# Optimization experiments

Measured on AMD Instinct MI355X. Metric: run time of the kernel, lower is better.

## Reference

```python
import jax, jax.numpy as jnp
import numpy as np

B, C3, H3, W3 = 8, 512, 24, 24
C5, H5, W5 = 256, 96, 96
GRIDS = (6, 3, 2, 1)
GROUPS = 2


def conv2d(x, w):
    # stride-1 'same' conv (matches torch autopad k//2 for odd k), NCHW/OIHW
    return jax.lax.conv_general_dilated(x, w, (1, 1), 'SAME',
                                        dimension_numbers=('NCHW', 'OIHW', 'NCHW'))


def conv_bn_silu(x, w):
    # ultralytics-style Conv = Conv2d(bias=False) + BatchNorm2d + SiLU.
    # BN in eval with default running stats (mean=0, var=1, gamma=1, beta=0) is identity.
    return jax.nn.silu(conv2d(x, w))


def psp(x):
    # adaptive_avg_pool2d to (g, g) for each grid; H,W divisible by all grids -> equal bins
    b, c, h, w = x.shape
    outs = []
    for g in GRIDS:
        outs.append(x.reshape(b, c, g, h // g, g, w // g).mean(axis=(3, 5)).reshape(b, c, g * g))
    return jnp.concatenate(outs, axis=2)  # [b, c, 36+9+4+1=50]


def resize_bilinear_ac(x, oh, ow):
    # F.interpolate(mode='bilinear', align_corners=True)
    n, c, h, w = x.shape
    ys = jnp.linspace(0.0, h - 1.0, oh)
    xs = jnp.linspace(0.0, w - 1.0, ow)
    y0 = jnp.clip(jnp.floor(ys).astype(jnp.int32), 0, h - 2)
    x0 = jnp.clip(jnp.floor(xs).astype(jnp.int32), 0, w - 2)
    wy = (ys - y0)[None, None, :, None]
    wx = (xs - x0)[None, None, None, :]
    xr = jnp.take(x, y0, axis=2) * (1 - wy) + jnp.take(x, y0 + 1, axis=2) * wy
    return jnp.take(xr, x0, axis=3) * (1 - wx) + jnp.take(xr, x0 + 1, axis=3) * wx


def grid_sample(img, grid):
    # F.grid_sample bilinear, align_corners=True, padding_mode='zeros'
    # img [N,C,H,W], grid [N,Ho,Wo,2] with (x,y) normalized coords
    n, c, h, w = img.shape
    gx = (grid[..., 0] + 1.0) * 0.5 * (w - 1)
    gy = (grid[..., 1] + 1.0) * 0.5 * (h - 1)
    x0 = jnp.floor(gx)
    y0 = jnp.floor(gy)
    wx1 = gx - x0
    wy1 = gy - y0
    flat = img.reshape(n, c, h * w)

    def gather(xi, yi, wgt):
        valid = (xi >= 0) & (xi <= w - 1) & (yi >= 0) & (yi <= h - 1)
        xc = jnp.clip(xi, 0, w - 1).astype(jnp.int32)
        yc = jnp.clip(yi, 0, h - 1).astype(jnp.int32)
        idx = (yc * w + xc).reshape(n, 1, -1)
        v = jnp.take_along_axis(flat, idx, axis=2).reshape(n, c, grid.shape[1], grid.shape[2])
        return v * (wgt * valid)[:, None]

    return (gather(x0, y0, (1 - wx1) * (1 - wy1)) + gather(x0 + 1, y0, wx1 * (1 - wy1))
            + gather(x0, y0 + 1, (1 - wx1) * wy1) + gather(x0 + 1, y0 + 1, wx1 * wy1))


def _w(key, shape):
    fan_in = int(np.prod(shape[1:]))
    return (jax.random.normal(key, shape, jnp.float32) / np.sqrt(fan_in)).astype(jnp.float32)


def setup_inputs() -> dict:
    key = jax.random.key(0)
    ks = jax.random.split(key, 17)
    return {
        'p3': jax.random.normal(ks[0], (B, C3, H3, W3), jnp.float32),
        'p5': jax.random.normal(ks[1], (B, C5, H5, W5), jnp.float32),
        # CFC_CRB
        'w_red': _w(ks[2], (C3, C3, 3, 3)),
        'wq': _w(ks[3], (32, C3, 1, 1)), 'bq': jnp.zeros((32,), jnp.float32),
        'wk': _w(ks[4], (32, C3)), 'bk': jnp.zeros((32,), jnp.float32),
        'wv': _w(ks[5], (C3, C3)), 'bv': jnp.zeros((C3,), jnp.float32),
        'la_w1': _w(ks[6], (C3 // 8, C3, 1, 1)),
        'la_w2': _w(ks[7], (C3, C3 // 8, 3, 3)),
        # SFC_G2
        'w32': _w(ks[8], (C5, C3, 3, 3)),
        'w8': _w(ks[9], (C5, C5, 3, 3)),
        'woff1': _w(ks[10], (64, 2 * C5, 1, 1)),
        'woff2': _w(ks[11], (GROUPS * 4 + 2, 64, 3, 3)),
    }


def reference(p3, p5, w_red, wq, bq, wk, bk, wv, bv, la_w1, la_w2, w32, w8, woff1, woff2):
    # ---------------- CFC_CRB ----------------
    x = conv_bn_silu(p3, w_red)                      # [b,512,h,w]
    b, c, h, w = x.shape
    q = conv2d(x, wq) + bq[None, :, None, None]       # [b,32,h,w]
    q = q.reshape(b, 32, h * w).transpose(0, 2, 1)    # [b,N,32]
    kfeat = psp(x)                                    # [b,512,50]
    k = jnp.einsum('oc,bcm->bom', wk, kfeat) + bk[None, :, None]   # [b,32,50]
    sim = jax.nn.softmax(jnp.einsum('bnc,bcm->bnm', q, k), axis=-1)  # [b,N,50]
    v = jnp.einsum('oc,bcm->bom', wv, kfeat) + bv[None, :, None]   # [b,512,50]
    context = jnp.einsum('bcm,bnm->bcn', v, sim).reshape(b, c, h, w)
    # LocalAttenModule: res1 * tanh(conv(context)) + res2
    mask = jnp.tanh(conv2d(conv_bn_silu(context, la_w1), la_w2))
    context = context * mask + context
    p3o = x + context                                 # [b,512,24,24]

    # ---------------- SFC_G2 ----------------
    sp = conv_bn_silu(p3o, w32)                       # [b,256,24,24]
    sp = resize_bilinear_ac(sp, H5, W5)               # [b,256,96,96]
    cp = conv_bn_silu(p5, w8)                         # [b,256,96,96]
    cr = conv2d(conv_bn_silu(jnp.concatenate([cp, sp], axis=1), woff1), woff2)  # [b,10,96,96]

    n = b
    spg = sp.reshape(n * GROUPS, -1, H5, W5)
    cpg = cp.reshape(n * GROUPS, -1, H5, W5)
    off_l = cr[:, 0:GROUPS * 2].reshape(n * GROUPS, 2, H5, W5)
    off_h = cr[:, GROUPS * 2:GROUPS * 4].reshape(n * GROUPS, 2, H5, W5)

    gx = jnp.linspace(-1.0, 1.0, W5)
    gy = jnp.linspace(-1.0, 1.0, H5)
    X, Y = jnp.meshgrid(gx, gy)                       # [H5,W5] each
    base = jnp.stack([X, Y], axis=-1)[None]           # [1,H5,W5,2] (x,y)
    norm = jnp.array([W5, H5], dtype=sp.dtype)
    grid_l = base + off_l.transpose(0, 2, 3, 1) / norm
    grid_h = base + off_h.transpose(0, 2, 3, 1) / norm

    cps = grid_sample(cpg, grid_l).reshape(n, -1, H5, W5)
    sps = grid_sample(spg, grid_h).reshape(n, -1, H5, W5)
    att = 1.0 + jnp.tanh(cr[:, GROUPS * 4:])          # [b,2,H,W]
    p5o = sps * att[:, 0:1] + cps * att[:, 1:2]
    return (p3o, p5o)
```

## Files before the change

### kernel.cpp

```cpp
#include <hip/hip_runtime.h>
#include <math.h>

#define DI __device__ __forceinline__

typedef __attribute__((ext_vector_type(8))) short bf16x8;
typedef __attribute__((ext_vector_type(4))) float f32x4;

DI float silu_f(float v) { return v / (1.f + __expf(-v)); }
DI float4 ld4(const float* p) { return *reinterpret_cast<const float4*>(p); }
DI void st4(float* p, const float4& v) { *reinterpret_cast<float4*>(p) = v; }
DI unsigned short f2bf(float f) {
    unsigned u = __float_as_uint(f);
    unsigned r = (u + 0x7FFFu + ((u >> 16) & 1u)) >> 16;
    return (unsigned short)r;
}
DI float bf2f(unsigned short u) { return __uint_as_float(((unsigned)u) << 16); }

DI void gload_lds16(const unsigned short* g, unsigned short* l) {
    __builtin_amdgcn_global_load_lds(
        (const __attribute__((address_space(1))) void*)g,
        (__attribute__((address_space(3))) void*)l, 16, 0, 0);
}

__global__ void pack_w2_kernel(const float* __restrict__ w, unsigned short* __restrict__ pk,
                               int Ci, int Co, int COG) {
    int idx = blockIdx.x * 256 + threadIdx.x;
    int total = Ci * Co * 9;
    if (idx >= total) return;
    int cc = idx & 31;
    int t = idx >> 5;
    int col = t % COG; t /= COG;
    int dydx = t % 9;  t /= 9;
    int nCoG = Co / COG;
    int cog = t % nCoG;
    int ch = t / nCoG;
    int co = cog * COG + col;
    pk[idx] = f2bf(w[((size_t)co * Ci + (ch << 5) + cc) * 9 + dydx]);
}

__global__ void pack_w1_kernel(const float* __restrict__ w, unsigned short* __restrict__ pk) {
    int idx = blockIdx.x * 256 + threadIdx.x;
    if (idx >= 32768) return;
    int cc = idx & 31;
    int col = (idx >> 5) & 63;
    int ch = idx >> 11;
    pk[idx] = f2bf(w[(size_t)col * 512 + (ch << 5) + cc]);
}

__global__ void zero_halo_kernel(unsigned short* __restrict__ pk, int P, int Hp, int Wp) {
    int border = 2 * Wp + 2 * (Hp - 2);
    int idx = blockIdx.x * 256 + threadIdx.x;
    if (idx >= P * border) return;
    int i = idx % border;
    int p = idx / border;
    int y, x;
    if (i < Wp) { y = 0; x = i; }
    else if (i < 2 * Wp) { y = Hp - 1; x = i - Wp; }
    else if (i < 2 * Wp + (Hp - 2)) { y = i - 2 * Wp + 1; x = 0; }
    else { y = i - 2 * Wp - (Hp - 2) + 1; x = Wp - 1; }
    unsigned short* d = pk + (((size_t)p * Hp + y) * Wp + x) * 32;
    uint4 z = make_uint4(0, 0, 0, 0);
    *(uint4*)&d[0] = z; *(uint4*)&d[8] = z; *(uint4*)&d[16] = z; *(uint4*)&d[24] = z;
}

__global__ void pack_in_pad_kernel(const float* __restrict__ in, unsigned short* __restrict__ pk,
                                   int Ci, int H, int W, int total) {
    int idx = blockIdx.x * 256 + threadIdx.x;
    if (idx >= total) return;
    const int nCh = Ci >> 5;
    const int HW = H * W;
    int cg = idx & 3;
    int t = idx >> 2;
    int pix = t % HW; t /= HW;
    int ch = t % nCh;
    int b = t / nCh;
    int y = pix / W, x = pix % W;
    const float* src = in + ((size_t)b * Ci + (ch << 5) + (cg << 3)) * HW + pix;
    unsigned p[4];
#pragma unroll
    for (int j = 0; j < 4; ++j) {
        float v0 = src[(size_t)(2 * j) * HW];
        float v1 = src[(size_t)(2 * j + 1) * HW];
        p[j] = (unsigned)f2bf(v0) | ((unsigned)f2bf(v1) << 16);
    }
    size_t dst = (((size_t)b * nCh + ch) * (H + 2) + (y + 1)) * (W + 2) + (x + 1);
    *(uint4*)&pk[dst * 32 + (cg << 3)] = make_uint4(p[0], p[1], p[2], p[3]);
}

template <int TH, int TW, int BF, int WCO, int FUSE, int OUTPK, int OUTPAD, int DBUF>
__global__ void __launch_bounds__(256)
conv3x3_mfma3(const unsigned short* __restrict__ pin, const unsigned short* __restrict__ wpk,
              float* __restrict__ out, unsigned short* __restrict__ outpk,
              int B, int Ci, int Co, int H, int W,
              const float* __restrict__ ctx, const float* __restrict__ xres) {
    static_assert(TH * TW == 4 * BF * 16, "tile px = 4 waves * BF frags * 16");
    constexpr int COG = WCO * 16;
    constexpr int TWH = TW + 2;
    constexpr int HP = (TH + 2) * TWH;
    constexpr int NG = HP * 4;
    constexpr int NIT = (NG + 255) / 256;
    static_assert(NG % 8 == 0, "granules divisible by 8");
    __shared__ __align__(16) unsigned short lin[NG * 8 * (DBUF + 1)];

    const int nTx = W / TW, nTy = H / TH, nCoG = Co / COG;
    const int Wp = W + 2, Hp = H + 2;
    const int nwg = gridDim.x;
    int wg = (blockIdx.x & 7) * (nwg >> 3) + (blockIdx.x >> 3);
    const int cog = wg % nCoG; wg /= nCoG;
    const int tx = wg % nTx;   wg /= nTx;
    const int ty = wg % nTy;
    const int b = wg / nTy;
    const int ox = tx * TW, oy = ty * TH, co0 = cog * COG;

    const int tid = threadIdx.x;
    const int lane = tid & 63;
    const int l15 = lane & 15, g = lane >> 4;
    const int wpx = (tid >> 6) * (BF * 16);

    int rr[BF], cc_[BF];
#pragma unroll
    for (int bf = 0; bf < BF; ++bf) {
        int px = wpx + bf * 16 + l15;
        rr[bf] = px / TW;
        cc_[bf] = px % TW;
    }

    f32x4 acc[WCO][BF];
#pragma unroll
    for (int af = 0; af < WCO; ++af)
#pragma unroll
        for (int bf = 0; bf < BF; ++bf) acc[af][bf] = {};

    const int nCh = Ci >> 5;
    const size_t HWs = (size_t)H * W;
    const size_t HpWp = (size_t)Hp * Wp;

    auto stage = [&](int ch, int buf) {
        const unsigned short* srcb = pin + ((size_t)b * nCh + ch) * HpWp * 32;
        unsigned short* dst = lin + buf * (NG * 8);
#pragma unroll
        for (int it = 0; it < NIT; ++it) {
            int s = it * 256 + tid;
            if (s < NG) {
                int e = s ^ ((s >> 3) & 7);
                int hp = e >> 2, cgp = e & 3;
                int hy = hp / TWH, hx = hp - hy * TWH;
                gload_lds16(srcb + ((size_t)(oy + hy) * Wp + (ox + hx)) * 32 + (cgp << 3),
                            &dst[(s & ~63) << 3]);
            }
        }
    };
    auto compute = [&](int ch, int buf) {
        const unsigned short* src = lin + buf * (NG * 8);
        const unsigned short* wbase =
            wpk + ((((size_t)ch * nCoG + cog) * 9) * COG + l15) * 32 + (g << 3);
#pragma unroll
        for (int dy = 0; dy < 3; ++dy) {
#pragma unroll
            for (int dx = 0; dx < 3; ++dx) {
                const int dydx = dy * 3 + dx;
                bf16x8 a[WCO];
#pragma unroll
                for (int af = 0; af < WCO; ++af)
                    a[af] = *(const bf16x8*)(wbase + ((size_t)dydx * COG + af * 16) * 32);
                bf16x8 bb[BF];
#pragma unroll
                for (int bf = 0; bf < BF; ++bf) {
                    int pxh = (rr[bf] + dy) * TWH + cc_[bf] + dx;
                    int eg = (pxh << 2) | g;
                    int slot = eg ^ ((eg >> 3) & 7);
                    bb[bf] = *(const bf16x8*)&src[slot << 3];
                }
#pragma unroll
                for (int af = 0; af < WCO; ++af)
#pragma unroll
                    for (int bf = 0; bf < BF; ++bf)
                        acc[af][bf] = __builtin_amdgcn_mfma_f32_16x16x32_bf16(
                            a[af], bb[bf], acc[af][bf], 0, 0, 0);
            }
        }
    };

    if (DBUF) {
        stage(0, 0);
        __syncthreads();
        for (int ch = 0; ch < nCh; ++ch) {
            if (ch + 1 < nCh) stage(ch + 1, (ch + 1) & 1);
            compute(ch, ch & 1);
            __syncthreads();
        }
    } else {
        for (int ch = 0; ch < nCh; ++ch) {
            stage(ch, 0);
            __syncthreads();
            compute(ch, 0);
            __syncthreads();
        }
    }

    const int nChO = Co >> 5;
    const size_t opitch = OUTPAD ? (size_t)(H + 2) * (W + 2) : HWs;
#pragma unroll
    for (int af = 0; af < WCO; ++af) {
#pragma unroll
        for (int bf = 0; bf < BF; ++bf) {
            int px = wpx + bf * 16 + l15;
            int y = oy + px / TW, x = ox + px % TW;
            size_t pixg = (size_t)y * W + x;
            int coB = co0 + af * 16 + (g << 2);
            float vv[4];
#pragma unroll
            for (int r4 = 0; r4 < 4; ++r4) {
                float v = acc[af][bf][r4];
                if (FUSE == 1) v = silu_f(v);
                else if (FUSE == 2) {
                    size_t base = ((size_t)b * Co + coB + r4) * HWs + pixg;
                    v = xres[base] + ctx[base] * (1.f + tanhf(v));
                }
                vv[r4] = v;
            }
            if (OUTPK != 1) {
#pragma unroll
                for (int r4 = 0; r4 < 4; ++r4)
                    out[((size_t)b * Co + coB + r4) * HWs + pixg] = vv[r4];
            }
            if (OUTPK >= 1) {
                ushort4 s;
                s.x = f2bf(vv[0]); s.y = f2bf(vv[1]); s.z = f2bf(vv[2]); s.w = f2bf(vv[3]);
                size_t opix = OUTPAD ? ((size_t)(y + 1) * (W + 2) + (x + 1)) : pixg;
                *(ushort4*)&outpk[(((size_t)b * nChO + (coB >> 5)) * opitch + opix) * 32
                                  + (coB & 31)] = s;
            }
        }
    }
}

__global__ void __launch_bounds__(256)
cat_mfma(const unsigned short* __restrict__ cp_pk, const unsigned short* __restrict__ sp_pk,
         const unsigned short* __restrict__ wpk, unsigned short* __restrict__ outpk) {
    __shared__ __align__(16) unsigned short lin1[128 * 36];
    const int nwg = gridDim.x;
    int wg = (blockIdx.x & 7) * (nwg >> 3) + (blockIdx.x >> 3);
    int mt = wg % 72;
    int b = wg / 72;
    int m0 = mt * 128;
    const int tid = threadIdx.x;
    const int wave = tid >> 6, lane = tid & 63;
    const int l15 = lane & 15, g = lane >> 4;
    const int wpx = wave * 32;

    f32x4 acc[4][2];
#pragma unroll
    for (int af = 0; af < 4; ++af)
#pragma unroll
        for (int bf = 0; bf < 2; ++bf) acc[af][bf] = {};

    for (int ch = 0; ch < 16; ++ch) {
        const unsigned short* src = (ch < 8)
            ? cp_pk + (((size_t)b * 8 + ch) * 9216 + m0) * 32
            : sp_pk + (((size_t)b * 8 + ch - 8) * 9216 + m0) * 32;
#pragma unroll
        for (int it = 0; it < 2; ++it) {
            int e = tid + it * 256;
            int px = e >> 2, cg = e & 3;
            *(uint4*)&lin1[px * 36 + (cg << 3)] = *(const uint4*)&src[px * 32 + (cg << 3)];
        }
        __syncthreads();
        const unsigned short* wb = wpk + ((size_t)ch * 64 + l15) * 32 + g * 8;
        bf16x8 a[4];
#pragma unroll
        for (int af = 0; af < 4; ++af)
            a[af] = *(const bf16x8*)(wb + (af * 16) * 32);
        bf16x8 bb[2];
#pragma unroll
        for (int bf = 0; bf < 2; ++bf)
            bb[bf] = *(const bf16x8*)&lin1[(wpx + bf * 16 + l15) * 36 + g * 8];
#pragma unroll
        for (int af = 0; af < 4; ++af)
#pragma unroll
            for (int bf = 0; bf < 2; ++bf)
                acc[af][bf] = __builtin_amdgcn_mfma_f32_16x16x32_bf16(
                    a[af], bb[bf], acc[af][bf], 0, 0, 0);
        __syncthreads();
    }
#pragma unroll
    for (int af = 0; af < 4; ++af) {
#pragma unroll
        for (int bf = 0; bf < 2; ++bf) {
            int m = m0 + wpx + bf * 16 + l15;
            int o = af * 16 + (g << 2);
            ushort4 s;
            s.x = f2bf(silu_f(acc[af][bf][0]));
            s.y = f2bf(silu_f(acc[af][bf][1]));
            s.z = f2bf(silu_f(acc[af][bf][2]));
            s.w = f2bf(silu_f(acc[af][bf][3]));
            *(ushort4*)&outpk[(((size_t)b * 2 + (o >> 5)) * 9216 + m) * 32 + (o & 31)] = s;
        }
    }
}

DI void gs_params(int x, int y, float ox, float oy, float4* w, int2* p) {
    const float S = 47.5f / 96.f;
    float px = x + ox * S;
    float py = y + oy * S;
    float fx0 = floorf(px), fy0 = floorf(py);
    float wx = px - fx0, wy = py - fy0;
    float vx0 = (fx0 >= 0.f && fx0 <= 95.f) ? 1.f : 0.f;
    float vx1 = (fx0 >= -1.f && fx0 <= 94.f) ? 1.f : 0.f;
    float vy0 = (fy0 >= 0.f && fy0 <= 95.f) ? 1.f : 0.f;
    float vy1 = (fy0 >= -1.f && fy0 <= 94.f) ? 1.f : 0.f;
    int x0 = (int)fminf(fmaxf(fx0, 0.f), 95.f);
    int x1 = (int)fminf(fmaxf(fx0 + 1.f, 0.f), 95.f);
    int y0 = (int)fminf(fmaxf(fy0, 0.f), 95.f);
    int y1 = (int)fminf(fmaxf(fy0 + 1.f, 0.f), 95.f);
    w->x = (1.f - wx) * (1.f - wy) * vx0 * vy0;
    w->y = wx * (1.f - wy) * vx1 * vy0;
    w->z = (1.f - wx) * wy * vx0 * vy1;
    w->w = wx * wy * vx1 * vy1;
    *p = make_int2(x0 | (x1 << 16), y0 | (y1 << 16));
}

template <int TH, int TW, int CO_BLK, int CO_T, int CIC, int FUSE>
__global__ void __launch_bounds__(576)
conv3x3_kernel(const unsigned short* __restrict__ in, const float* __restrict__ wgt,
               float* __restrict__ out, int B, int Ci, int Co, int H, int W,
               float4* __restrict__ wpar, int2* __restrict__ ipk,
               float2* __restrict__ attp) {
    constexpr int TWH = TW + 2;
    constexpr int TWP = TW + 3;
    constexpr int SPAT = TH * (TW / 4);
    __shared__ float lin[CIC][TH + 2][TWP];
    __shared__ float wls[CIC][9][CO_BLK];
    __shared__ float crs[10][TH * TW + 1];

    const int nTx = W / TW, nTy = H / TH;
    const int nCoG = (Co + CO_BLK - 1) / CO_BLK;
    int bid = blockIdx.x;
    const int cog = bid % nCoG; bid /= nCoG;
    const int tx = bid % nTx;   bid /= nTx;
    const int ty = bid % nTy;
    const int b = bid / nTy;
    const int ox = tx * TW, oy = ty * TH;
    const int co0 = cog * CO_BLK;

    const int tid = threadIdx.x;
    const int cot = tid / SPAT;
    const int sp = tid % SPAT;
    const int r = sp / (TW / 4);
    const int cg = sp % (TW / 4);
    const int nChI = Ci >> 5;

    float acc[4][4];
#pragma unroll
    for (int i = 0; i < 4; ++i)
#pragma unroll
        for (int j = 0; j < 4; ++j) acc[i][j] = 0.f;

    for (int ci0 = 0; ci0 < Ci; ci0 += CIC) {
        for (int e = tid; e < CIC * (TH + 2) * TWH; e += SPAT * CO_T) {
            int xx = e % TWH;
            int yy = (e / TWH) % (TH + 2);
            int cc = e / (TWH * (TH + 2));
            int gy = oy - 1 + yy, gx = ox - 1 + xx;
            float v = 0.f;
            if (gy >= 0 && gy < H && gx >= 0 && gx < W) {
                int ci = ci0 + cc;
                v = bf2f(in[(((size_t)b * nChI + (ci >> 5)) * H * W
                             + (size_t)gy * W + gx) * 32 + (ci & 31)]);
            }
            lin[cc][yy][xx] = v;
        }
        for (int e = tid; e < CIC * 9 * CO_BLK; e += SPAT * CO_T) {
            int col = e % CO_BLK;
            int k = (e / CO_BLK) % 9;
            int cc = e / (CO_BLK * 9);
            int co = co0 + col;
            float v = 0.f;
            if (co < Co) v = wgt[((size_t)co * Ci + ci0 + cc) * 9 + k];
            wls[cc][k][col] = v;
        }
        __syncthreads();
#pragma unroll
        for (int cc = 0; cc < CIC; ++cc) {
            float v0[3][6];
#pragma unroll
            for (int ky = 0; ky < 3; ++ky)
#pragma unroll
                for (int u = 0; u < 6; ++u)
                    v0[ky][u] = lin[cc][r + ky][cg * 4 + u];
#pragma unroll
            for (int ky = 0; ky < 3; ++ky)
#pragma unroll
                for (int kx = 0; kx < 3; ++kx) {
                    const float4 w4 = ld4(&wls[cc][ky * 3 + kx][cot * 4]);
                    const float wv_[4] = {w4.x, w4.y, w4.z, w4.w};
#pragma unroll
                    for (int i = 0; i < 4; ++i)
#pragma unroll
                        for (int j = 0; j < 4; ++j)
                            acc[i][j] = fmaf(wv_[i], v0[ky][kx + j], acc[i][j]);
                }
        }
        __syncthreads();
    }
    if (FUSE == 3) {
#pragma unroll
        for (int i = 0; i < 4; ++i) {
            int co = co0 + cot * 4 + i;
            if (co >= 10) continue;
#pragma unroll
            for (int j = 0; j < 4; ++j)
                crs[co][r * TW + cg * 4 + j] = acc[i][j];
        }
        __syncthreads();
        for (int e = tid; e < TH * TW; e += SPAT * CO_T) {
            int xx = ox + (e % TW), yy = oy + (e / TW);
            int pixg = yy * 96 + xx;
            float4 w; int2 p;
#pragma unroll
            for (int g2 = 0; g2 < 2; ++g2) {
                gs_params(xx, yy, crs[2 * g2][e], crs[2 * g2 + 1][e], &w, &p);
                size_t el = ((size_t)g2 * 8 + b) * 9216 + pixg;
                wpar[el] = w; ipk[el] = p;
                gs_params(xx, yy, crs[4 + 2 * g2][e], crs[5 + 2 * g2][e], &w, &p);
                size_t eh = ((size_t)(2 + g2) * 8 + b) * 9216 + pixg;
                wpar[eh] = w; ipk[eh] = p;
            }
            float2 at;
            at.x = 1.f + tanhf(crs[8][e]);
            at.y = 1.f + tanhf(crs[9][e]);
            attp[(size_t)b * 9216 + pixg] = at;
        }
    } else {
        const int y = oy + r;
        const int xb = ox + cg * 4;
#pragma unroll
        for (int i = 0; i < 4; ++i) {
            int co = co0 + cot * 4 + i;
            if (co >= Co) continue;
            size_t base = (((size_t)b * Co + co) * H + y) * W + xb;
            float4 res;
            res.x = acc[i][0]; res.y = acc[i][1]; res.z = acc[i][2]; res.w = acc[i][3];
            st4(&out[base], res);
        }
    }
}

template <int ACT, int PK>
__global__ void __launch_bounds__(256)
gemm_om(const float* __restrict__ W, const float* __restrict__ bias,
        const float* __restrict__ in, float* __restrict__ out,
        unsigned short* __restrict__ pko,
        int B, int C, int O, int M, int nOt, int nMt) {
    __shared__ float xs[32][66];
    __shared__ float wls[64][33];
    int bid = blockIdx.x;
    int mt = bid % nMt; bid /= nMt;
    int ot = bid % nOt;
    int b  = bid / nOt;
    int o0 = ot * 64, m0 = mt * 64;
    int tid = threadIdx.x;
    int m_t = tid & 15, o_g = tid >> 4;
    float acc[4][4];
#pragma unroll
    for (int i = 0; i < 4; ++i)
#pragma unroll
        for (int j = 0; j < 4; ++j) acc[i][j] = 0.f;

    for (int c0 = 0; c0 < C; c0 += 32) {
#pragma unroll
        for (int it = 0; it < 8; ++it) {
            int e = tid + it * 256;
            int mm = e & 63, cc = e >> 6;
            float v = 0.f;
            if (m0 + mm < M) v = in[((size_t)b * C + c0 + cc) * M + m0 + mm];
            xs[cc][mm] = v;
        }
#pragma unroll
        for (int it = 0; it < 8; ++it) {
            int e = tid + it * 256;
            int cc = e & 31, ol = e >> 5;
            float v = 0.f;
            if (o0 + ol < O) v = W[(size_t)(o0 + ol) * C + c0 + cc];
            wls[ol][cc] = v;
        }
        __syncthreads();
#pragma unroll
        for (int cc = 0; cc < 32; ++cc) {
            float xv[4], wv[4];
#pragma unroll
            for (int j = 0; j < 4; ++j) xv[j] = xs[cc][j * 16 + m_t];
#pragma unroll
            for (int i = 0; i < 4; ++i) wv[i] = wls[o_g * 4 + i][cc];
#pragma unroll
            for (int i = 0; i < 4; ++i)
#pragma unroll
                for (int j = 0; j < 4; ++j)
                    acc[i][j] = fmaf(wv[i], xv[j], acc[i][j]);
        }
        __syncthreads();
    }
#pragma unroll
    for (int i = 0; i < 4; ++i) {
        int o = o0 + o_g * 4 + i;
        if (o >= O) continue;
        float bv = bias ? bias[o] : 0.f;
#pragma unroll
        for (int j = 0; j < 4; ++j) {
            int m = m0 + j * 16 + m_t;
            if (m >= M) continue;
            float v = acc[i][j] + bv;
            if (ACT == 1) v = silu_f(v);
            if (PK) {
                int yy = m / 24, xx = m % 24;
                pko[(((size_t)b * (O >> 5) + (o >> 5)) * 676
                     + (size_t)(yy + 1) * 26 + (xx + 1)) * 32 + (o & 31)] = f2bf(v);
            } else {
                out[((size_t)b * O + o) * M + m] = v;
            }
        }
    }
}

__global__ void __launch_bounds__(256)
gemm_kv(const float* __restrict__ wk, const float* __restrict__ bk,
        const float* __restrict__ wv, const float* __restrict__ bv,
        const float* __restrict__ in, float* __restrict__ kv) {
    __shared__ float xs[32][66];
    __shared__ float wls[64][33];
    const int O = 544, M = 50, C = 512;
    int bid = blockIdx.x;
    int ot = bid % 9;
    int b  = bid / 9;
    int o0 = ot * 64;
    int tid = threadIdx.x;
    int m_t = tid & 15, o_g = tid >> 4;
    float acc[4][4];
#pragma unroll
    for (int i = 0; i < 4; ++i)
#pragma unroll
        for (int j = 0; j < 4; ++j) acc[i][j] = 0.f;

    for (int c0 = 0; c0 < C; c0 += 32) {
#pragma unroll
        for (int it = 0; it < 8; ++it) {
            int e = tid + it * 256;
            int mm = e & 63, cc = e >> 6;
            float v = 0.f;
            if (mm < M) v = in[((size_t)b * C + c0 + cc) * M + mm];
            xs[cc][mm] = v;
        }
#pragma unroll
        for (int it = 0; it < 8; ++it) {
            int e = tid + it * 256;
            int cc = e & 31, ol = e >> 5;
            int o = o0 + ol;
            float v = 0.f;
            if (o < 32) v = wk[(size_t)o * C + c0 + cc];
            else if (o < O) v = wv[(size_t)(o - 32) * C + c0 + cc];
            wls[ol][cc] = v;
        }
        __syncthreads();
#pragma unroll
        for (int cc = 0; cc < 32; ++cc) {
            float xv[4], wv_[4];
#pragma unroll
            for (int j = 0; j < 4; ++j) xv[j] = xs[cc][j * 16 + m_t];
#pragma unroll
            for (int i = 0; i < 4; ++i) wv_[i] = wls[o_g * 4 + i][cc];
#pragma unroll
            for (int i = 0; i < 4; ++i)
#pragma unroll
                for (int j = 0; j < 4; ++j)
                    acc[i][j] = fmaf(wv_[i], xv[j], acc[i][j]);
        }
        __syncthreads();
    }
#pragma unroll
    for (int i = 0; i < 4; ++i) {
        int o = o0 + o_g * 4 + i;
        if (o >= O) continue;
        float bvv = (o < 32) ? bk[o] : bv[o - 32];
#pragma unroll
        for (int j = 0; j < 4; ++j) {
            int m = j * 16 + m_t;
            if (m >= M) continue;
            kv[((size_t)b * O + o) * M + m] = acc[i][j] + bvv;
        }
    }
}

__global__ void psp_kernel(const float* __restrict__ x, float* __restrict__ kf) {
    __shared__ float pl[576];
    int bc = blockIdx.x;
    const float* xp = x + (size_t)bc * 576;
    for (int e = threadIdx.x; e < 576; e += 64) pl[e] = xp[e];
    __syncthreads();
    int m = threadIdx.x;
    if (m < 50) {
        int g, i0;
        if (m < 36)      { g = 6; i0 = m; }
        else if (m < 45) { g = 3; i0 = m - 36; }
        else if (m < 49) { g = 2; i0 = m - 45; }
        else             { g = 1; i0 = 0; }
        int bs = 24 / g;
        int by = i0 / g, bx = i0 % g;
        float s = 0.f;
        for (int yy = 0; yy < bs; ++yy)
            for (int xx = 0; xx < bs; ++xx)
                s += pl[(by * bs + yy) * 24 + bx * bs + xx];
        kf[(size_t)bc * 50 + m] = s / (float)(bs * bs);
    }
}

__global__ void __launch_bounds__(256)
sim_kernel(const float* __restrict__ q, const float* __restrict__ kv,
           float* __restrict__ simg) {
    __shared__ float qs[32][65];
    __shared__ float ks[32][52];
    __shared__ float sm[64][52];
    int b = blockIdx.x / 9, n0 = (blockIdx.x % 9) * 64;
    int tid = threadIdx.x;
    for (int e = tid; e < 32 * 64; e += 256) {
        int c = e >> 6, n = e & 63;
        qs[c][n] = q[((size_t)b * 32 + c) * 576 + n0 + n];
    }
    for (int e = tid; e < 32 * 50; e += 256) {
        int c = e / 50, m = e % 50;
        ks[c][m] = kv[((size_t)b * 544 + c) * 50 + m];
    }
    __syncthreads();
    for (int e = tid; e < 64 * 50; e += 256) {
        int n = e / 50, m = e % 50;
        float s = 0.f;
#pragma unroll
        for (int c = 0; c < 32; ++c) s = fmaf(qs[c][n], ks[c][m], s);
        sm[n][m] = s;
    }
    __syncthreads();
    if (tid < 64) {
        float mx = -1e30f;
        for (int m = 0; m < 50; ++m) mx = fmaxf(mx, sm[tid][m]);
        float sum = 0.f;
        for (int m = 0; m < 50; ++m) {
            float e2 = __expf(sm[tid][m] - mx);
            sm[tid][m] = e2;
            sum += e2;
        }
        float inv = 1.f / sum;
        for (int m = 0; m < 50; ++m) sm[tid][m] *= inv;
    }
    __syncthreads();
    for (int e = tid; e < 64 * 50; e += 256) {
        int n = e / 50, m = e % 50;
        simg[((size_t)b * 576 + n0 + n) * 50 + m] = sm[n][m];
    }
}

__global__ void __launch_bounds__(256)
ctx_kernel(const float* __restrict__ kv, const float* __restrict__ simg,
           float* __restrict__ ctx) {
    __shared__ float vs[128][54];
    __shared__ float ss[64][54];
    int blk = blockIdx.x;
    int ct = blk & 3; blk >>= 2;
    int nt = blk % 9;
    int b = blk / 9;
    int c0 = ct * 128, n0 = nt * 64;
    int tid = threadIdx.x;
    for (int e = tid; e < 128 * 50; e += 256) {
        int c = e / 50, m = e % 50;
        vs[c][m] = kv[((size_t)b * 544 + 32 + c0 + c) * 50 + m];
    }
    for (int e = tid; e < 64 * 50; e += 256) {
        int n = e / 50, m = e % 50;
        ss[n][m] = simg[((size_t)b * 576 + n0 + n) * 50 + m];
    }
    __syncthreads();
    int n_t = tid & 15;
    int c_t = tid >> 4;
    float acc[8][4];
#pragma unroll
    for (int i = 0; i < 8; ++i)
#pragma unroll
        for (int j = 0; j < 4; ++j) acc[i][j] = 0.f;
    for (int m = 0; m < 50; ++m) {
        float sv[4];
#pragma unroll
        for (int j = 0; j < 4; ++j) sv[j] = ss[j * 16 + n_t][m];
#pragma unroll
        for (int i = 0; i < 8; ++i) {
            float vv = vs[c_t * 8 + i][m];
#pragma unroll
            for (int j = 0; j < 4; ++j) acc[i][j] = fmaf(vv, sv[j], acc[i][j]);
        }
    }
#pragma unroll
    for (int i = 0; i < 8; ++i)
#pragma unroll
        for (int j = 0; j < 4; ++j)
            ctx[((size_t)b * 512 + c0 + c_t * 8 + i) * 576 + n0 + j * 16 + n_t] = acc[i][j];
}

__global__ void upsample2_kernel(const float* __restrict__ in, unsigned short* __restrict__ outpk) {
    int idx = blockIdx.x * 256 + threadIdx.x;
    if (idx >= 8 * 8 * 4 * 9216) return;
    int cg = idx & 3;
    int t = idx >> 2;
    int pix = t % 9216; t /= 9216;
    int ch = t & 7;
    int b = t >> 3;
    int x = pix % 96, y = pix / 96;
    float fy = y * (23.f / 95.f);
    float fx = x * (23.f / 95.f);
    int y0 = (int)fy; if (y0 > 22) y0 = 22;
    int x0 = (int)fx; if (x0 > 22) x0 = 22;
    float wy = fy - y0, wx = fx - x0;
    const float* base = in + ((size_t)b * 256 + ch * 32 + cg * 8) * 576 + y0 * 24 + x0;
    unsigned short s[8];
#pragma unroll
    for (int j = 0; j < 8; ++j) {
        const float* ip = base + (size_t)j * 576;
        float a = ip[0], bb = ip[1], c = ip[24], d = ip[25];
        float l = a * (1.f - wy) + c * wy;
        float r = bb * (1.f - wy) + d * wy;
        s[j] = f2bf(l * (1.f - wx) + r * wx);
    }
    *(uint4*)&outpk[(((size_t)b * 8 + ch) * 9216 + pix) * 32 + cg * 8] =
        make_uint4((unsigned)s[0] | ((unsigned)s[1] << 16),
                   (unsigned)s[2] | ((unsigned)s[3] << 16),
                   (unsigned)s[4] | ((unsigned)s[5] << 16),
                   (unsigned)s[6] | ((unsigned)s[7] << 16));
}

__global__ void __launch_bounds__(256)
gsample3_kernel(const unsigned short* __restrict__ cp_pk, const unsigned short* __restrict__ sp_pk,
                const float4* __restrict__ wpar, const int2* __restrict__ ipk,
                const float2* __restrict__ attp, float* __restrict__ p5o) {
    int idx = blockIdx.x * 256 + threadIdx.x;
    if (idx >= 8 * 32 * 9216) return;
    int pix = idx % 9216;
    int cb = (idx / 9216) & 31;
    int b = idx / (9216 * 32);
    int c0 = cb * 8;
    int g = c0 >> 7, ch = c0 >> 5, coff = c0 & 31;
    size_t el = ((size_t)g * 8 + b) * 9216 + pix;
    size_t eh = ((size_t)(2 + g) * 8 + b) * 9216 + pix;
    float4 wl = wpar[el]; int2 pl = ipk[el];
    float4 wh = wpar[eh]; int2 ph = ipk[eh];
    float2 at = attp[(size_t)b * 9216 + pix];
    int l00 = (pl.y & 0xffff) * 96 + (pl.x & 0xffff);
    int l01 = (pl.y & 0xffff) * 96 + (pl.x >> 16);
    int l10 = (pl.y >> 16) * 96 + (pl.x & 0xffff);
    int l11 = (pl.y >> 16) * 96 + (pl.x >> 16);
    int h00 = (ph.y & 0xffff) * 96 + (ph.x & 0xffff);
    int h01 = (ph.y & 0xffff) * 96 + (ph.x >> 16);
    int h10 = (ph.y >> 16) * 96 + (ph.x & 0xffff);
    int h11 = (ph.y >> 16) * 96 + (ph.x >> 16);
    const unsigned short* cb0 = cp_pk + (((size_t)b * 8 + ch) * 9216) * 32 + coff;
    const unsigned short* sb0 = sp_pk + (((size_t)b * 8 + ch) * 9216) * 32 + coff;
    ushort4 tc0 = *(const ushort4*)&cb0[(size_t)l00 * 32];
    ushort4 tc0b = *(const ushort4*)&cb0[(size_t)l00 * 32 + 4];
    ushort4 tc1 = *(const ushort4*)&cb0[(size_t)l01 * 32];
    ushort4 tc1b = *(const ushort4*)&cb0[(size_t)l01 * 32 + 4];
    ushort4 tc2 = *(const ushort4*)&cb0[(size_t)l10 * 32];
    ushort4 tc2b = *(const ushort4*)&cb0[(size_t)l10 * 32 + 4];
    ushort4 tc3 = *(const ushort4*)&cb0[(size_t)l11 * 32];
    ushort4 tc3b = *(const ushort4*)&cb0[(size_t)l11 * 32 + 4];
    ushort4 ts0 = *(const ushort4*)&sb0[(size_t)h00 * 32];
    ushort4 ts0b = *(const ushort4*)&sb0[(size_t)h00 * 32 + 4];
    ushort4 ts1 = *(const ushort4*)&sb0[(size_t)h01 * 32];
    ushort4 ts1b = *(const ushort4*)&sb0[(size_t)h01 * 32 + 4];
    ushort4 ts2 = *(const ushort4*)&sb0[(size_t)h10 * 32];
    ushort4 ts2b = *(const ushort4*)&sb0[(size_t)h10 * 32 + 4];
    ushort4 ts3 = *(const ushort4*)&sb0[(size_t)h11 * 32];
    ushort4 ts3b = *(const ushort4*)&sb0[(size_t)h11 * 32 + 4];
    const unsigned short* c0a = (const unsigned short*)&tc0;
    const unsigned short* c0bp = (const unsigned short*)&tc0b;
    const unsigned short* c1a = (const unsigned short*)&tc1;
    const unsigned short* c1bp = (const unsigned short*)&tc1b;
    const unsigned short* c2a = (const unsigned short*)&tc2;
    const unsigned short* c2bp = (const unsigned short*)&tc2b;
    const unsigned short* c3a = (const unsigned short*)&tc3;
    const unsigned short* c3bp = (const unsigned short*)&tc3b;
    const unsigned short* s0a = (const unsigned short*)&ts0;
    const unsigned short* s0bp = (const unsigned short*)&ts0b;
    const unsigned short* s1a = (const unsigned short*)&ts1;
    const unsigned short* s1bp = (const unsigned short*)&ts1b;
    const unsigned short* s2a = (const unsigned short*)&ts2;
    const unsigned short* s2bp = (const unsigned short*)&ts2b;
    const unsigned short* s3a = (const unsigned short*)&ts3;
    const unsigned short* s3bp = (const unsigned short*)&ts3b;
    float* op = p5o + ((size_t)b * 256 + c0) * 9216 + pix;
#pragma unroll
    for (int i = 0; i < 8; ++i) {
        unsigned short v0 = (i < 4) ? c0a[i] : c0bp[i - 4];
        unsigned short v1 = (i < 4) ? c1a[i] : c1bp[i - 4];
        unsigned short v2 = (i < 4) ? c2a[i] : c2bp[i - 4];
        unsigned short v3 = (i < 4) ? c3a[i] : c3bp[i - 4];
        float cps = wl.x * bf2f(v0) + wl.y * bf2f(v1) + wl.z * bf2f(v2) + wl.w * bf2f(v3);
        unsigned short u0 = (i < 4) ? s0a[i] : s0bp[i - 4];
        unsigned short u1 = (i < 4) ? s1a[i] : s1bp[i - 4];
        unsigned short u2 = (i < 4) ? s2a[i] : s2bp[i - 4];
        unsigned short u3 = (i < 4) ? s3a[i] : s3bp[i - 4];
        float sps = wh.x * bf2f(u0) + wh.y * bf2f(u1) + wh.z * bf2f(u2) + wh.w * bf2f(u3);
        op[(size_t)i * 9216] = sps * at.x + cps * at.y;
    }
}

extern "C" void kernel_launch(void* const* d_in, const int* in_sizes, int n_in,
                              void* d_out, int out_size, void* d_ws, size_t ws_size,
                              hipStream_t stream) {
    const float* p3    = (const float*)d_in[0];
    const float* p5    = (const float*)d_in[1];
    const float* w_red = (const float*)d_in[2];
    const float* wq    = (const float*)d_in[3];
    const float* bq    = (const float*)d_in[4];
    const float* wk    = (const float*)d_in[5];
    const float* bk    = (const float*)d_in[6];
    const float* wv    = (const float*)d_in[7];
    const float* bv    = (const float*)d_in[8];
    const float* la_w1 = (const float*)d_in[9];
    const float* la_w2 = (const float*)d_in[10];
    const float* w32   = (const float*)d_in[11];
    const float* w8    = (const float*)d_in[12];
    const float* woff1 = (const float*)d_in[13];
    const float* woff2 = (const float*)d_in[14];

    float* out = (float*)d_out;
    float* p3o = out;
    float* p5o = out + 2359296;

    float* ws = (float*)d_ws;
    float* x_   = ws + 0;
    float* ctx  = ws + 2359296;
    float* q    = ws + 4718592;
    float* kf   = ws + 4866048;
    float* kv   = ws + 5070848;
    unsigned short* la1_pk = (unsigned short*)(ws + 5288448);
    float* sp24 = ws + 5461504;
    float4* wpar = (float4*)(ws + 6641152);
    int2*   ipk  = (int2*)(ws + 7820800);
    float2* attp = (float2*)(ws + 8410624);
    float* simg = ws + 8558080;
    unsigned short* sp96_pk = (unsigned short*)(ws + 8788480);
    unsigned short* cp_pk   = (unsigned short*)(ws + 18225664);
    unsigned short* p5_pk   = (unsigned short*)(ws + 27662848);
    unsigned short* p3_pk   = (unsigned short*)(ws + 37497344);
    unsigned short* wred_pk = (unsigned short*)(ws + 38881792);
    unsigned short* w32_pk  = (unsigned short*)(ws + 40061440);
    unsigned short* w8_pk   = (unsigned short*)(ws + 40651264);
    unsigned short* wla2_pk = (unsigned short*)(ws + 40946176);
    unsigned short* woff1_pk= (unsigned short*)(ws + 41093632);
    unsigned short* t64_pk  = (unsigned short*)(ws + 0);

    zero_halo_kernel<<<dim3((64 * 388 + 255) / 256), dim3(256), 0, stream>>>(p5_pk, 64, 98, 98);
    zero_halo_kernel<<<dim3((128 * 100 + 255) / 256), dim3(256), 0, stream>>>(p3_pk, 128, 26, 26);
    zero_halo_kernel<<<dim3((16 * 100 + 255) / 256), dim3(256), 0, stream>>>(la1_pk, 16, 26, 26);

    pack_w2_kernel<<<dim3(2359296 / 256), dim3(256), 0, stream>>>(w_red, wred_pk, 512, 512, 32);
    pack_w2_kernel<<<dim3(1179648 / 256), dim3(256), 0, stream>>>(w32, w32_pk, 512, 256, 16);
    pack_w2_kernel<<<dim3(589824 / 256), dim3(256), 0, stream>>>(w8, w8_pk, 256, 256, 64);
    pack_w2_kernel<<<dim3(294912 / 256), dim3(256), 0, stream>>>(la_w2, wla2_pk, 64, 512, 32);
    pack_w1_kernel<<<dim3(128), dim3(256), 0, stream>>>(woff1, woff1_pk);
    pack_in_pad_kernel<<<dim3(9216), dim3(256), 0, stream>>>(p5, p5_pk, 256, 96, 96, 2359296);
    pack_in_pad_kernel<<<dim3(1152), dim3(256), 0, stream>>>(p3, p3_pk, 512, 24, 24, 294912);

    conv3x3_mfma3<16, 16, 4, 4, 1, 1, 0, 0><<<dim3(1152), dim3(256), 0, stream>>>(
        p5_pk, w8_pk, nullptr, cp_pk, 8, 256, 256, 96, 96, nullptr, nullptr);
    conv3x3_mfma3<8, 24, 3, 2, 1, 0, 0, 0><<<dim3(384), dim3(256), 0, stream>>>(
        p3_pk, wred_pk, x_, nullptr, 8, 512, 512, 24, 24, nullptr, nullptr);
    gemm_om<0, 0><<<dim3(72), dim3(256), 0, stream>>>(
        wq, bq, x_, q, nullptr, 8, 512, 32, 576, 1, 9);
    psp_kernel<<<dim3(8 * 512), dim3(64), 0, stream>>>(x_, kf);
    gemm_kv<<<dim3(72), dim3(256), 0, stream>>>(wk, bk, wv, bv, kf, kv);
    sim_kernel<<<dim3(72), dim3(256), 0, stream>>>(q, kv, simg);
    ctx_kernel<<<dim3(288), dim3(256), 0, stream>>>(kv, simg, ctx);
    gemm_om<1, 1><<<dim3(72), dim3(256), 0, stream>>>(
        la_w1, nullptr, ctx, nullptr, la1_pk, 8, 512, 64, 576, 1, 9);
    conv3x3_mfma3<8, 24, 3, 2, 2, 2, 1, 0><<<dim3(384), dim3(256), 0, stream>>>(
        la1_pk, wla2_pk, p3o, p3_pk, 8, 64, 512, 24, 24, ctx, x_);
    conv3x3_mfma3<8, 24, 3, 1, 1, 0, 0, 0><<<dim3(384), dim3(256), 0, stream>>>(
        p3_pk, w32_pk, sp24, nullptr, 8, 512, 256, 24, 24, nullptr, nullptr);
    upsample2_kernel<<<dim3(9216), dim3(256), 0, stream>>>(sp24, sp96_pk);
    cat_mfma<<<dim3(576), dim3(256), 0, stream>>>(cp_pk, sp96_pk, woff1_pk, t64_pk);
    conv3x3_kernel<8, 32, 12, 3, 4, 3><<<dim3(288), dim3(192), 0, stream>>>(
        t64_pk, woff2, nullptr, 8, 64, 10, 96, 96, wpar, ipk, attp);
    gsample3_kernel<<<dim3(9216), dim3(256), 0, stream>>>(
        cp_pk, sp96_pk, wpar, ipk, attp, p5o);
}
```

Before: 781.5 us.

## Give each wave a private LDS halo tile and drop block-wide barriers

The 3x3 MFMA conv kernel now has each of the four waves stage its own row strip plus halo into a private LDS region. It then waits only on its own vector-memory counter instead of calling __syncthreads twice per input-channel chunk. This removes block-level barrier stalls and lets waves progress independently. The cost is that halo rows are loaded redundantly by adjacent waves, which means more global traffic and LDS use. The double-buffer template option is also gone, so staging and compute within a wave are no longer overlapped.

```diff
diff --git a/kernel.cpp b/kernel.cpp
--- a/kernel.cpp
+++ b/kernel.cpp
@@ -87,20 +87,22 @@
     *(uint4*)&pk[dst * 32 + (cg << 3)] = make_uint4(p[0], p[1], p[2], p[3]);
 }
 
-template <int TH, int TW, int BF, int WCO, int FUSE, int OUTPK, int OUTPAD, int DBUF>
+template <int TH, int TW, int BF, int WCO, int FUSE, int OUTPK, int OUTPAD>
 __global__ void __launch_bounds__(256)
-conv3x3_mfma3(const unsigned short* __restrict__ pin, const unsigned short* __restrict__ wpk,
+conv3x3_mfma5(const unsigned short* __restrict__ pin, const unsigned short* __restrict__ wpk,
               float* __restrict__ out, unsigned short* __restrict__ outpk,
               int B, int Ci, int Co, int H, int W,
               const float* __restrict__ ctx, const float* __restrict__ xres) {
     static_assert(TH * TW == 4 * BF * 16, "tile px = 4 waves * BF frags * 16");
     constexpr int COG = WCO * 16;
-    constexpr int TWH = TW + 2;
-    constexpr int HP = (TH + 2) * TWH;
-    constexpr int NG = HP * 4;
-    constexpr int NIT = (NG + 255) / 256;
-    static_assert(NG % 8 == 0, "granules divisible by 8");
-    __shared__ __align__(16) unsigned short lin[NG * 8 * (DBUF + 1)];
+    constexpr int WROWS = (BF * 16) / TW;
+    static_assert(WROWS * TW == BF * 16, "wave px must be whole rows");
+    static_assert(TH == 4 * WROWS, "4 waves cover TH rows");
+    constexpr int RW = TW + 2;
+    constexpr int RHP = (WROWS + 2) * RW;
+    constexpr int NGW = RHP * 4;
+    constexpr int NITW = (NGW + 63) / 64;
+    __shared__ __align__(16) unsigned short lin[4 * NGW * 8];
 
     const int nTx = W / TW, nTy = H / TH, nCoG = Co / COG;
     const int Wp = W + 2, Hp = H + 2;
@@ -113,16 +115,18 @@
     const int ox = tx * TW, oy = ty * TH, co0 = cog * COG;
 
     const int tid = threadIdx.x;
-    const int lane = tid & 63;
+    const int wave = tid >> 6, lane = tid & 63;
     const int l15 = lane & 15, g = lane >> 4;
-    const int wpx = (tid >> 6) * (BF * 16);
-
-    int rr[BF], cc_[BF];
+    const int wpx = wave * (BF * 16);
+    const int wrow0 = wave * WROWS;
+    unsigned short* wlds = lin + (size_t)wave * NGW * 8;
+
+    int rloc[BF], cc_[BF];
 #pragma unroll
     for (int bf = 0; bf < BF; ++bf) {
-        int px = wpx + bf * 16 + l15;
-        rr[bf] = px / TW;
-        cc_[bf] = px % TW;
+        int t = bf * 16 + l15;
+        rloc[bf] = t / TW;
+        cc_[bf] = t % TW;
     }
 
     f32x4 acc[WCO][BF];
@@ -135,66 +139,52 @@
     const size_t HWs = (size_t)H * W;
     const size_t HpWp = (size_t)Hp * Wp;
 
-    auto stage = [&](int ch, int buf) {
-        const unsigned short* srcb = pin + ((size_t)b * nCh + ch) * HpWp * 32;
-        unsigned short* dst = lin + buf * (NG * 8);
-#pragma unroll
-        for (int it = 0; it < NIT; ++it) {
-            int s = it * 256 + tid;
-            if (s < NG) {
-                int e = s ^ ((s >> 3) & 7);
-                int hp = e >> 2, cgp = e & 3;
-                int hy = hp / TWH, hx = hp - hy * TWH;
-                gload_lds16(srcb + ((size_t)(oy + hy) * Wp + (ox + hx)) * 32 + (cgp << 3),
-                            &dst[(s & ~63) << 3]);
+    for (int ch = 0; ch < nCh; ++ch) {
+        {
+            const unsigned short* srcb = pin + ((size_t)b * nCh + ch) * HpWp * 32;
+#pragma unroll
+            for (int it = 0; it < NITW; ++it) {
+                int s = it * 64 + lane;
+                if (s < NGW) {
+                    int e = s ^ ((s >> 3) & 7);
+                    int hp = e >> 2, cgp = e & 3;
+                    int hy = hp / RW, hx = hp - hy * RW;
+                    gload_lds16(srcb + ((size_t)(oy + wrow0 + hy) * Wp + (ox + hx)) * 32
+                                     + (cgp << 3),
+                                &wlds[(s & ~63) << 3]);
+                }
             }
         }
-    };
-    auto compute = [&](int ch, int buf) {
-        const unsigned short* src = lin + buf * (NG * 8);
-        const unsigned short* wbase =
-            wpk + ((((size_t)ch * nCoG + cog) * 9) * COG + l15) * 32 + (g << 3);
-#pragma unroll
-        for (int dy = 0; dy < 3; ++dy) {
-#pragma unroll
-            for (int dx = 0; dx < 3; ++dx) {
-                const int dydx = dy * 3 + dx;
-                bf16x8 a[WCO];
-#pragma unroll
-                for (int af = 0; af < WCO; ++af)
-                    a[af] = *(const bf16x8*)(wbase + ((size_t)dydx * COG + af * 16) * 32);
-                bf16x8 bb[BF];
-#pragma unroll
-                for (int bf = 0; bf < BF; ++bf) {
-                    int pxh = (rr[bf] + dy) * TWH + cc_[bf] + dx;
-                    int eg = (pxh << 2) | g;
-                    int slot = eg ^ ((eg >> 3) & 7);
-                    bb[bf] = *(const bf16x8*)&src[slot << 3];
+        asm volatile("s_waitcnt vmcnt(0)" ::: "memory");
+        __builtin_amdgcn_sched_barrier(0);
+        {
+            const unsigned short* wbase =
+                wpk + ((((size_t)ch * nCoG + cog) * 9) * COG + l15) * 32 + (g << 3);
+#pragma unroll
+            for (int dy = 0; dy < 3; ++dy) {
+#pragma unroll
+                for (int dx = 0; dx < 3; ++dx) {
+                    const int dydx = dy * 3 + dx;
+                    bf16x8 a[WCO];
+#pragma unroll
+                    for (int af = 0; af < WCO; ++af)
+                        a[af] = *(const bf16x8*)(wbase + ((size_t)dydx * COG + af * 16) * 32);
+                    bf16x8 bb[BF];
+#pragma unroll
+                    for (int bf = 0; bf < BF; ++bf) {
+                        int hp = (rloc[bf] + dy) * RW + cc_[bf] + dx;
+                        int eg = (hp << 2) | g;
+                        int slot = eg ^ ((eg >> 3) & 7);
+                        bb[bf] = *(const bf16x8*)&wlds[slot << 3];
+                    }
+#pragma unroll
+                    for (int af = 0; af < WCO; ++af)
+#pragma unroll
+                        for (int bf = 0; bf < BF; ++bf)
+                            acc[af][bf] = __builtin_amdgcn_mfma_f32_16x16x32_bf16(
+                                a[af], bb[bf], acc[af][bf], 0, 0, 0);
                 }
-#pragma unroll
-                for (int af = 0; af < WCO; ++af)
-#pragma unroll
-                    for (int bf = 0; bf < BF; ++bf)
-                        acc[af][bf] = __builtin_amdgcn_mfma_f32_16x16x32_bf16(
-                            a[af], bb[bf], acc[af][bf], 0, 0, 0);
             }
-        }
-    };
-
-    if (DBUF) {
-        stage(0, 0);
-        __syncthreads();
-        for (int ch = 0; ch < nCh; ++ch) {
-            if (ch + 1 < nCh) stage(ch + 1, (ch + 1) & 1);
-            compute(ch, ch & 1);
-            __syncthreads();
-        }
-    } else {
-        for (int ch = 0; ch < nCh; ++ch) {
-            stage(ch, 0);
-            __syncthreads();
-            compute(ch, 0);
-            __syncthreads();
         }
     }
 
@@ -204,8 +194,7 @@
     for (int af = 0; af < WCO; ++af) {
 #pragma unroll
         for (int bf = 0; bf < BF; ++bf) {
-            int px = wpx + bf * 16 + l15;
-            int y = oy + px / TW, x = ox + px % TW;
+            int y = oy + wrow0 + rloc[bf], x = ox + cc_[bf];
             size_t pixg = (size_t)y * W + x;
             int coB = co0 + af * 16 + (g << 2);
             float vv[4];
@@ -866,9 +855,9 @@
     pack_in_pad_kernel<<<dim3(9216), dim3(256), 0, stream>>>(p5, p5_pk, 256, 96, 96, 2359296);
     pack_in_pad_kernel<<<dim3(1152), dim3(256), 0, stream>>>(p3, p3_pk, 512, 24, 24, 294912);
 
-    conv3x3_mfma3<16, 16, 4, 4, 1, 1, 0, 0><<<dim3(1152), dim3(256), 0, stream>>>(
+    conv3x3_mfma5<16, 16, 4, 4, 1, 1, 0><<<dim3(1152), dim3(256), 0, stream>>>(
         p5_pk, w8_pk, nullptr, cp_pk, 8, 256, 256, 96, 96, nullptr, nullptr);
-    conv3x3_mfma3<8, 24, 3, 2, 1, 0, 0, 0><<<dim3(384), dim3(256), 0, stream>>>(
+    conv3x3_mfma5<8, 24, 3, 2, 1, 0, 0><<<dim3(384), dim3(256), 0, stream>>>(
         p3_pk, wred_pk, x_, nullptr, 8, 512, 512, 24, 24, nullptr, nullptr);
     gemm_om<0, 0><<<dim3(72), dim3(256), 0, stream>>>(
         wq, bq, x_, q, nullptr, 8, 512, 32, 576, 1, 9);
@@ -878,9 +867,9 @@
     ctx_kernel<<<dim3(288), dim3(256), 0, stream>>>(kv, simg, ctx);
     gemm_om<1, 1><<<dim3(72), dim3(256), 0, stream>>>(
         la_w1, nullptr, ctx, nullptr, la1_pk, 8, 512, 64, 576, 1, 9);
-    conv3x3_mfma3<8, 24, 3, 2, 2, 2, 1, 0><<<dim3(384), dim3(256), 0, stream>>>(
+    conv3x3_mfma5<8, 24, 3, 2, 2, 2, 1><<<dim3(384), dim3(256), 0, stream>>>(
         la1_pk, wla2_pk, p3o, p3_pk, 8, 64, 512, 24, 24, ctx, x_);
-    conv3x3_mfma3<8, 24, 3, 1, 1, 0, 0, 0><<<dim3(384), dim3(256), 0, stream>>>(
+    conv3x3_mfma5<8, 24, 3, 1, 1, 0, 0><<<dim3(384), dim3(256), 0, stream>>>(
         p3_pk, w32_pk, sp24, nullptr, 8, 512, 256, 24, 24, nullptr, nullptr);
     upsample2_kernel<<<dim3(9216), dim3(256), 0, stream>>>(sp24, sp96_pk);
     cat_mfma<<<dim3(576), dim3(256), 0, stream>>>(cp_pk, sp96_pk, woff1_pk, t64_pk);
```

Result: slower. 813.0 us (+4.0%).
